# Kernel optimization log

Measured on AMD Instinct MI355X. Metric: run time of the kernel, lower is better.

The kernel has to match this reference:

```python
import jax, jax.numpy as jnp
import numpy as np

N_NODES = 100000


def gcn_conv(x, src, dst, W, b):
    """PyG GCNConv: add self-loops, symmetric D^-1/2 (A+I) D^-1/2 normalization.
    x: [N, Fin]; src/dst: [E'] (self-loops already appended); W: [Fin, Fout]; b: [Fout].
    """
    xw = x @ W  # [N, Fout]
    ones = jnp.ones(dst.shape[0], dtype=x.dtype)
    deg = jax.ops.segment_sum(ones, dst, num_segments=N_NODES)  # in-degree incl. self-loop
    dinv = jnp.where(deg > 0, jax.lax.rsqrt(deg), 0.0)
    norm = dinv[src] * dinv[dst]  # [E']
    msg = xw[src] * norm[:, None]  # gather + scale
    out = jax.ops.segment_sum(msg, dst, num_segments=N_NODES)  # scatter-add
    return out + b


def setup_inputs() -> dict:
    key = jax.random.key(0)
    ks = jax.random.split(key, 12)
    hidden = 64
    E = 1600000
    x_node = jax.random.normal(ks[0], (N_NODES, 1), dtype=jnp.float32)
    edge_index = jax.random.randint(ks[1], (2, E), 0, N_NODES, dtype=jnp.int64)

    def glorot(k, fan_in, fan_out):
        lim = float(np.sqrt(6.0 / (fan_in + fan_out)))
        return jax.random.uniform(k, (fan_in, fan_out), jnp.float32, -lim, lim)

    W1 = glorot(ks[2], 1, hidden)
    b1 = jnp.zeros((hidden,), jnp.float32)
    W2 = glorot(ks[3], hidden, hidden)
    b2 = jnp.zeros((hidden,), jnp.float32)
    W3 = glorot(ks[4], hidden, hidden)
    b3 = jnp.zeros((hidden,), jnp.float32)
    W4 = glorot(ks[5], hidden, 1)
    b4 = jnp.zeros((1,), jnp.float32)
    return {"x_node": x_node, "edge_index": edge_index,
            "W1": W1, "b1": b1, "W2": W2, "b2": b2,
            "W3": W3, "b3": b3, "W4": W4, "b4": b4}


def reference(x_node, edge_index, W1, b1, W2, b2, W3, b3, W4, b4):
    # Append self-loops once (shared by both GCN layers, as PyG does per-layer with identical result)
    loops = jnp.arange(N_NODES, dtype=edge_index.dtype)
    src = jnp.concatenate([edge_index[0], loops])
    dst = jnp.concatenate([edge_index[1], loops])

    h = jax.nn.silu(gcn_conv(x_node, src, dst, W1, b1))
    h = jax.nn.silu(gcn_conv(h, src, dst, W2, b2))
    h = jax.nn.silu(h @ W3 + b3)
    return h @ W4 + b4  # [N, 1]
```

## Files before the change

### kernel.cpp

```cpp
#include <hip/hip_runtime.h>
#include <math.h>

#define N_NODES 100000
#define NPB    392
#define NBUCK  256
#define CAP    7168
#define CHUNKA 4096

#define NCHEB  12
#define SMAX   6.0f

__device__ __forceinline__ float silu_f(float x) {
    return x * __builtin_amdgcn_rcpf(1.0f + __builtin_amdgcn_exp2f(-1.442695041f * x));
}

__global__ __launch_bounds__(512) void k_bucket(const int* __restrict__ src,
                                                const int* __restrict__ dst,
                                                int* __restrict__ gcur,
                                                unsigned int* __restrict__ buf,
                                                const float* __restrict__ W1,
                                                const float* __restrict__ b1,
                                                float* __restrict__ cheb, int E) {
    __shared__ unsigned hist[256];
    __shared__ unsigned gbase[256];
    __shared__ unsigned lcur[256];
    const int t = threadIdx.x;
    if (t < 256) hist[t] = 0;
    __syncthreads();
    const int e0 = blockIdx.x * CHUNKA;
    const int e1 = min(e0 + CHUNKA, E);

    int sR[8], dR[8], bR[8];
#pragma unroll
    for (int q = 0; q < 8; ++q) {
        int e = e0 + t + q * 512;
        if (e < e1) {
            dR[q] = dst[e];
            sR[q] = src[e];
            bR[q] = dR[q] / NPB;
            atomicAdd(&hist[bR[q]], 1u);
        } else bR[q] = -1;
    }
    __syncthreads();
    if (t < 256) {
        unsigned v = hist[t];
        gbase[t] = v ? (unsigned)atomicAdd(&gcur[t], (int)v) : 0u;
        lcur[t] = 0;
    }
    __syncthreads();
#pragma unroll
    for (int q = 0; q < 8; ++q) {
        if (bR[q] >= 0) {
            int b = bR[q];
            unsigned gp = gbase[b] + atomicAdd(&lcur[b], 1u);
            if (gp < CAP)
                buf[(size_t)b * CAP + gp] =
                    ((unsigned)sR[q] << 9) | (unsigned)(dR[q] - b * NPB);
        }
    }

    if (blockIdx.x == 0 && t < 64) {
        int f = t;
        float w = W1[f], b = b1[f];
        float g[NCHEB], th[NCHEB];
        const float pi = 3.14159265358979f;
#pragma unroll
        for (int j = 0; j < NCHEB; ++j) {
            th[j] = (j + 0.5f) * (pi / NCHEB);
            float S = SMAX * __cosf(th[j]);
            float y = fmaf(w, S, b);
            g[j] = y / (1.0f + expf(-y));
        }
#pragma unroll
        for (int k = 0; k < NCHEB; ++k) {
            float s = 0.f;
#pragma unroll
            for (int j = 0; j < NCHEB; ++j)
                s += g[j] * __cosf((float)k * th[j]);
            cheb[k * 64 + f] = s * ((k == 0) ? (1.0f / NCHEB) : (2.0f / NCHEB));
        }
    }
}

__global__ __launch_bounds__(512) void k_deg(const int* __restrict__ gcur,
                                             const unsigned int* __restrict__ buf,
                                             const float* __restrict__ x,
                                             const float* __restrict__ W2,
                                             const float* __restrict__ cheb,
                                             float* __restrict__ cw2,
                                             int* __restrict__ cnt,
                                             float* __restrict__ dinv,
                                             float* __restrict__ xs, int N) {
    __shared__ unsigned hist[512];
    const int b = blockIdx.x, t = threadIdx.x;
    const int cb = min(gcur[b], CAP);
    const unsigned int* bb = buf + (size_t)b * CAP;
    hist[t] = 0;
    __syncthreads();
    for (int i = t; i < cb; i += 512) atomicAdd(&hist[bb[i] & 511u], 1u);
    __syncthreads();
    const int n0 = b * NPB;
    const int np = min(N - n0, NPB);
    if (t < np) {
        cnt[n0 + t] = (int)hist[t];
        float dv = rsqrtf((float)(hist[t] + 1u));
        dinv[n0 + t] = dv;
        xs[n0 + t] = x[n0 + t] * dv;
    }

    if (b == 0 && t < 64) {
        const int f2 = t;
        float acc[NCHEB];
#pragma unroll
        for (int k = 0; k < NCHEB; ++k) acc[k] = 0.f;
        for (int f = 0; f < 64; ++f) {
            float w = W2[f * 64 + f2];
#pragma unroll
            for (int k = 0; k < NCHEB; ++k)
                acc[k] = fmaf(cheb[k * 64 + f], w, acc[k]);
        }
#pragma unroll
        for (int k = 0; k < NCHEB; ++k) cw2[k * 64 + f2] = acc[k];
    }
}

__global__ __launch_bounds__(512) void k_csr3(const int* __restrict__ gcur,
                                              const unsigned int* __restrict__ buf,
                                              const int* __restrict__ cnt,
                                              const float* __restrict__ xs,
                                              const float* __restrict__ dinv,
                                              int* __restrict__ rowptr,
                                              int* __restrict__ csr,
                                              float2* __restrict__ sd, int N) {
    __shared__ unsigned cur[512];
    __shared__ unsigned wtot[8];
    __shared__ unsigned lsrc[CAP];
    __shared__ float    lval[CAP];
    const int b = blockIdx.x, t = threadIdx.x;
    const int lane = t & 63, wid = t >> 6;
    const int cb = min(gcur[b], CAP);
    const unsigned int* bb = buf + (size_t)b * CAP;
    const int n0 = b * NPB;
    const int node = n0 + t;

    unsigned v = (t < NPB && node < N) ? (unsigned)cnt[node] : 0u;
    unsigned sc = v;
#pragma unroll
    for (int off = 1; off < 64; off <<= 1) {
        unsigned y = __shfl_up(sc, off, 64);
        if (lane >= off) sc += y;
    }
    if (lane == 63) wtot[wid] = sc;
    __syncthreads();
    unsigned add = 0;
    for (int w = 0; w < wid; ++w) add += wtot[w];
    unsigned ex = sc - v + add;
    cur[t] = ex;
    __syncthreads();

    int i = t;
    for (; i + 1536 < cb; i += 2048) {
        unsigned p0 = bb[i], p1 = bb[i + 512], p2 = bb[i + 1024], p3 = bb[i + 1536];
        float a0 = xs[p0 >> 9], a1 = xs[p1 >> 9], a2 = xs[p2 >> 9], a3 = xs[p3 >> 9];
        unsigned q0 = atomicAdd(&cur[p0 & 511u], 1u);
        unsigned q1 = atomicAdd(&cur[p1 & 511u], 1u);
        unsigned q2 = atomicAdd(&cur[p2 & 511u], 1u);
        unsigned q3 = atomicAdd(&cur[p3 & 511u], 1u);
        lsrc[q0] = p0 >> 9; lval[q0] = a0;
        lsrc[q1] = p1 >> 9; lval[q1] = a1;
        lsrc[q2] = p2 >> 9; lval[q2] = a2;
        lsrc[q3] = p3 >> 9; lval[q3] = a3;
    }
    for (; i < cb; i += 512) {
        unsigned p = bb[i];
        float a = xs[p >> 9];
        unsigned q = atomicAdd(&cur[p & 511u], 1u);
        lsrc[q] = p >> 9; lval[q] = a;
    }
    __syncthreads();

    for (int j = t; j < cb; j += 512) csr[(size_t)b * CAP + j] = lsrc[j];

    if (t < NPB && node < N) {
        int deg = (int)v;
        int st  = (int)ex;
        rowptr[node] = b * CAP + st;
        float sum = 0.f;
        for (int j = 0; j < deg; ++j) sum += lval[st + j];
        float dv = dinv[node];
        sd[node] = make_float2((sum + xs[node]) * dv, dv);
    }
}

__global__ __launch_bounds__(512) void k_momlp(
    const int* __restrict__ rowptr, const int* __restrict__ cnt,
    const int* __restrict__ csr, const float2* __restrict__ sd,
    const float* __restrict__ cw2,
    const float* __restrict__ b2,
    const float* __restrict__ W3, const float* __restrict__ b3,
    const float* __restrict__ W4, const float* __restrict__ b4,
    float* __restrict__ out, int N)
{
    __shared__ float sA[64 * 65];
    __shared__ float sM[64 * 13];
    __shared__ float sD[64];
    __shared__ float sP[8 * 64];

    const int t = threadIdx.x;
    const int lane = t & 63;
    const int wid  = __builtin_amdgcn_readfirstlane(t >> 6);
    const int nbase = blockIdx.x * 64;
    const int loc = t >> 3, sub = t & 7;
    const int i = nbase + loc;

    int start = 0, deg = 0;
    float2 self = make_float2(0.f, 0.f);
    if (i < N) {
        start = rowptr[i];
        deg   = cnt[i];
        self  = sd[i];
    }

    float m[NCHEB];
    {
        float d = (sub == 0) ? self.y : 0.f;
        float tt = fminf(fmaxf(self.x * (1.0f / SMAX), -1.f), 1.f);
        float t2 = tt + tt, Tm = 1.f, Tc = tt;
        m[0] = d;
        m[1] = d * tt;
#pragma unroll
        for (int k = 2; k < NCHEB; ++k) {
            float Tn = fmaf(t2, Tc, -Tm);
            m[k] = d * Tn;
            Tm = Tc; Tc = Tn;
        }
    }

    int uu[4];
    float2 sv[4];
#pragma unroll
    for (int q = 0; q < 4; ++q) {
        int j = sub + 8 * q;
        uu[q] = (j < deg) ? csr[start + j] : -1;
    }
#pragma unroll
    for (int q = 0; q < 4; ++q)
        sv[q] = (uu[q] >= 0) ? sd[uu[q]] : make_float2(0.f, 0.f);
#pragma unroll
    for (int q = 0; q < 4; ++q) {
        if (uu[q] >= 0) {
            float d = sv[q].y;
            float tt = fminf(fmaxf(sv[q].x * (1.0f / SMAX), -1.f), 1.f);
            float t2 = tt + tt, Tm = 1.f, Tc = tt;
            m[0] += d;
            m[1] = fmaf(d, tt, m[1]);
#pragma unroll
            for (int k = 2; k < NCHEB; ++k) {
                float Tn = fmaf(t2, Tc, -Tm);
                m[k] = fmaf(d, Tn, m[k]);
                Tm = Tc; Tc = Tn;
            }
        }
    }
    for (int j = sub + 32; j < deg; j += 8) {
        int u = csr[start + j];
        float2 su = sd[u];
        float d = su.y;
        float tt = fminf(fmaxf(su.x * (1.0f / SMAX), -1.f), 1.f);
        float t2 = tt + tt, Tm = 1.f, Tc = tt;
        m[0] += d;
        m[1] = fmaf(d, tt, m[1]);
#pragma unroll
        for (int k = 2; k < NCHEB; ++k) {
            float Tn = fmaf(t2, Tc, -Tm);
            m[k] = fmaf(d, Tn, m[k]);
            Tm = Tc; Tc = Tn;
        }
    }
#pragma unroll
    for (int k = 0; k < NCHEB; ++k) {
        m[k] += __shfl_xor(m[k], 1, 64);
        m[k] += __shfl_xor(m[k], 2, 64);
        m[k] += __shfl_xor(m[k], 4, 64);
    }
    sM[loc * 13 + sub] = m[sub];
    if (sub < 4) sM[loc * 13 + 8 + sub] = m[8 + sub];
    if (sub == 0) sD[loc] = self.y;

    float cw[NCHEB];
#pragma unroll
    for (int k = 0; k < NCHEB; ++k) cw[k] = cw2[k * 64 + lane];
    const float b2l = b2[lane];
    __syncthreads();

    const int r0 = wid * 8;
#pragma unroll
    for (int nl = 0; nl < 8; ++nl) {
        int row = r0 + nl;
        float acc = 0.f;
#pragma unroll
        for (int k = 0; k < NCHEB; ++k)
            acc = fmaf(cw[k], sM[row * 13 + k], acc);
        sA[row * 65 + lane] = silu_f(fmaf(sD[row], acc, b2l));
    }
    __syncthreads();

    const int f0 = wid * 8;
    float acc3[8];
#pragma unroll
    for (int j = 0; j < 8; ++j) acc3[j] = b3[f0 + j];
    for (int k = 0; k < 64; ++k) {
        float uv = sA[lane * 65 + k];
#pragma unroll
        for (int j = 0; j < 8; ++j)
            acc3[j] = fmaf(uv, W3[k * 64 + f0 + j], acc3[j]);
    }
    float part = 0.f;
#pragma unroll
    for (int j = 0; j < 8; ++j)
        part = fmaf(silu_f(acc3[j]), W4[f0 + j], part);
    sP[wid * 64 + lane] = part;
    __syncthreads();

    if (wid == 0) {
        int i2 = nbase + lane;
        if (i2 < N) {
            float s = sP[lane];
#pragma unroll
            for (int w = 1; w < 8; ++w) s += sP[w * 64 + lane];
            out[i2] = s + b4[0];
        }
    }
}

extern "C" void kernel_launch(void* const* d_in, const int* in_sizes, int n_in,
                              void* d_out, int out_size, void* d_ws, size_t ws_size,
                              hipStream_t stream) {
    const float* x  = (const float*)d_in[0];
    const int* edge = (const int*)d_in[1];
    const float* W1 = (const float*)d_in[2];
    const float* b1 = (const float*)d_in[3];
    const float* W2 = (const float*)d_in[4];
    const float* b2 = (const float*)d_in[5];
    const float* W3 = (const float*)d_in[6];
    const float* b3 = (const float*)d_in[7];
    const float* W4 = (const float*)d_in[8];
    const float* b4 = (const float*)d_in[9];
    float* out = (float*)d_out;

    const int N = N_NODES;
    const int E = in_sizes[1] / 2;
    const int* src = edge;
    const int* dst = edge + E;
    const int NCHUNK = (E + CHUNKA - 1) / CHUNKA;

    char* ws = (char*)d_ws;
    size_t off = 0;
    int*    gcur   = (int*)(ws + off);    off += 256 * 4;
    float*  dinv   = (float*)(ws + off);  off += (size_t)N * 4;
    float*  xs     = (float*)(ws + off);  off += (size_t)N * 4;
    int*    rowptr = (int*)(ws + off);    off += (size_t)N * 4;
    int*    cnt    = (int*)(ws + off);    off += (size_t)N * 4;
    float2* sd     = (float2*)(ws + off); off += (size_t)N * 8;
    float*  cheb   = (float*)(ws + off);  off += NCHEB * 64 * 4;
    float*  cw2    = (float*)(ws + off);  off += NCHEB * 64 * 4;
    unsigned int* buf = (unsigned int*)(ws + off); off += (size_t)NBUCK * CAP * 4;
    int*    csr    = (int*)(ws + off);    off += (size_t)NBUCK * CAP * 4;

    hipMemsetAsync(gcur, 0, 256 * 4, stream);

    k_bucket<<<NCHUNK, 512, 0, stream>>>(src, dst, gcur, buf, W1, b1, cheb, E);
    k_deg   <<<NBUCK, 512, 0, stream>>>(gcur, buf, x, W2, cheb, cw2, cnt, dinv, xs, N);
    k_csr3  <<<NBUCK, 512, 0, stream>>>(gcur, buf, cnt, xs, dinv,
                                        rowptr, csr, sd, N);
    k_momlp <<<(N + 63) / 64, 512, 0, stream>>>(rowptr, cnt, csr, sd, cw2,
                                                b2, W3, b3, W4, b4, out, N);
}
```

Baseline: 148.7 us.

## Fold degree counting into bucketing via global atomics and drop k_deg kernel

Per-node in-degree is now counted with a global atomicAdd in the bucketing kernel, so the separate degree-histogram kernel is removed. The CSR kernel recomputes the normalized source value from x and cnt on the fly, and also takes over the cw2 precompute. This removes one launch and one full pass over the bucket buffer, but adds about 1.7M global atomics spread across 100K counters and an extra gather of cnt per edge. The memset now also clears the count array.

After: 203.6 us. +36.9%, slower.

```diff
diff --git a/kernel.cpp b/kernel.cpp
--- a/kernel.cpp
+++ b/kernel.cpp
@@ -17,6 +17,7 @@
 __global__ __launch_bounds__(512) void k_bucket(const int* __restrict__ src,
                                                 const int* __restrict__ dst,
                                                 int* __restrict__ gcur,
+                                                int* __restrict__ cnt,
                                                 unsigned int* __restrict__ buf,
                                                 const float* __restrict__ W1,
                                                 const float* __restrict__ b1,
@@ -39,6 +40,7 @@
             sR[q] = src[e];
             bR[q] = dR[q] / NPB;
             atomicAdd(&hist[bR[q]], 1u);
+            atomicAdd(&cnt[dR[q]], 1);
         } else bR[q] = -1;
     }
     __syncthreads();
@@ -82,53 +84,13 @@
     }
 }
 
-__global__ __launch_bounds__(512) void k_deg(const int* __restrict__ gcur,
-                                             const unsigned int* __restrict__ buf,
-                                             const float* __restrict__ x,
-                                             const float* __restrict__ W2,
-                                             const float* __restrict__ cheb,
-                                             float* __restrict__ cw2,
-                                             int* __restrict__ cnt,
-                                             float* __restrict__ dinv,
-                                             float* __restrict__ xs, int N) {
-    __shared__ unsigned hist[512];
-    const int b = blockIdx.x, t = threadIdx.x;
-    const int cb = min(gcur[b], CAP);
-    const unsigned int* bb = buf + (size_t)b * CAP;
-    hist[t] = 0;
-    __syncthreads();
-    for (int i = t; i < cb; i += 512) atomicAdd(&hist[bb[i] & 511u], 1u);
-    __syncthreads();
-    const int n0 = b * NPB;
-    const int np = min(N - n0, NPB);
-    if (t < np) {
-        cnt[n0 + t] = (int)hist[t];
-        float dv = rsqrtf((float)(hist[t] + 1u));
-        dinv[n0 + t] = dv;
-        xs[n0 + t] = x[n0 + t] * dv;
-    }
-
-    if (b == 0 && t < 64) {
-        const int f2 = t;
-        float acc[NCHEB];
-#pragma unroll
-        for (int k = 0; k < NCHEB; ++k) acc[k] = 0.f;
-        for (int f = 0; f < 64; ++f) {
-            float w = W2[f * 64 + f2];
-#pragma unroll
-            for (int k = 0; k < NCHEB; ++k)
-                acc[k] = fmaf(cheb[k * 64 + f], w, acc[k]);
-        }
-#pragma unroll
-        for (int k = 0; k < NCHEB; ++k) cw2[k * 64 + f2] = acc[k];
-    }
-}
-
-__global__ __launch_bounds__(512) void k_csr3(const int* __restrict__ gcur,
+__global__ __launch_bounds__(512) void k_csr4(const int* __restrict__ gcur,
                                               const unsigned int* __restrict__ buf,
                                               const int* __restrict__ cnt,
-                                              const float* __restrict__ xs,
-                                              const float* __restrict__ dinv,
+                                              const float* __restrict__ x,
+                                              const float* __restrict__ W2,
+                                              const float* __restrict__ cheb,
+                                              float* __restrict__ cw2,
                                               int* __restrict__ rowptr,
                                               int* __restrict__ csr,
                                               float2* __restrict__ sd, int N) {
@@ -161,21 +123,28 @@
     int i = t;
     for (; i + 1536 < cb; i += 2048) {
         unsigned p0 = bb[i], p1 = bb[i + 512], p2 = bb[i + 1024], p3 = bb[i + 1536];
-        float a0 = xs[p0 >> 9], a1 = xs[p1 >> 9], a2 = xs[p2 >> 9], a3 = xs[p3 >> 9];
+        int s0 = p0 >> 9, s1 = p1 >> 9, s2 = p2 >> 9, s3 = p3 >> 9;
+        float x0 = x[s0], x1 = x[s1], x2 = x[s2], x3 = x[s3];
+        int c0 = cnt[s0], c1 = cnt[s1], c2 = cnt[s2], c3 = cnt[s3];
+        float a0 = x0 * rsqrtf((float)(c0 + 1));
+        float a1 = x1 * rsqrtf((float)(c1 + 1));
+        float a2 = x2 * rsqrtf((float)(c2 + 1));
+        float a3 = x3 * rsqrtf((float)(c3 + 1));
         unsigned q0 = atomicAdd(&cur[p0 & 511u], 1u);
         unsigned q1 = atomicAdd(&cur[p1 & 511u], 1u);
         unsigned q2 = atomicAdd(&cur[p2 & 511u], 1u);
         unsigned q3 = atomicAdd(&cur[p3 & 511u], 1u);
-        lsrc[q0] = p0 >> 9; lval[q0] = a0;
-        lsrc[q1] = p1 >> 9; lval[q1] = a1;
-        lsrc[q2] = p2 >> 9; lval[q2] = a2;
-        lsrc[q3] = p3 >> 9; lval[q3] = a3;
+        lsrc[q0] = (unsigned)s0; lval[q0] = a0;
+        lsrc[q1] = (unsigned)s1; lval[q1] = a1;
+        lsrc[q2] = (unsigned)s2; lval[q2] = a2;
+        lsrc[q3] = (unsigned)s3; lval[q3] = a3;
     }
     for (; i < cb; i += 512) {
         unsigned p = bb[i];
-        float a = xs[p >> 9];
+        int s = p >> 9;
+        float a = x[s] * rsqrtf((float)(cnt[s] + 1));
         unsigned q = atomicAdd(&cur[p & 511u], 1u);
-        lsrc[q] = p >> 9; lval[q] = a;
+        lsrc[q] = (unsigned)s; lval[q] = a;
     }
     __syncthreads();
 
@@ -185,10 +154,25 @@
         int deg = (int)v;
         int st  = (int)ex;
         rowptr[node] = b * CAP + st;
+        float dv = rsqrtf((float)(deg + 1));
         float sum = 0.f;
         for (int j = 0; j < deg; ++j) sum += lval[st + j];
-        float dv = dinv[node];
-        sd[node] = make_float2((sum + xs[node]) * dv, dv);
+        sd[node] = make_float2((sum + x[node] * dv) * dv, dv);
+    }
+
+    if (b == 0 && t < 64) {
+        const int f2 = t;
+        float acc[NCHEB];
+#pragma unroll
+        for (int k = 0; k < NCHEB; ++k) acc[k] = 0.f;
+        for (int f = 0; f < 64; ++f) {
+            float w = W2[f * 64 + f2];
+#pragma unroll
+            for (int k = 0; k < NCHEB; ++k)
+                acc[k] = fmaf(cheb[k * 64 + f], w, acc[k]);
+        }
+#pragma unroll
+        for (int k = 0; k < NCHEB; ++k) cw2[k * 64 + f2] = acc[k];
     }
 }
 
@@ -357,21 +341,18 @@
     char* ws = (char*)d_ws;
     size_t off = 0;
     int*    gcur   = (int*)(ws + off);    off += 256 * 4;
-    float*  dinv   = (float*)(ws + off);  off += (size_t)N * 4;
-    float*  xs     = (float*)(ws + off);  off += (size_t)N * 4;
+    int*    cnt    = (int*)(ws + off);    off += (size_t)N * 4;
     int*    rowptr = (int*)(ws + off);    off += (size_t)N * 4;
-    int*    cnt    = (int*)(ws + off);    off += (size_t)N * 4;
     float2* sd     = (float2*)(ws + off); off += (size_t)N * 8;
     float*  cheb   = (float*)(ws + off);  off += NCHEB * 64 * 4;
     float*  cw2    = (float*)(ws + off);  off += NCHEB * 64 * 4;
     unsigned int* buf = (unsigned int*)(ws + off); off += (size_t)NBUCK * CAP * 4;
     int*    csr    = (int*)(ws + off);    off += (size_t)NBUCK * CAP * 4;
 
-    hipMemsetAsync(gcur, 0, 256 * 4, stream);
-
-    k_bucket<<<NCHUNK, 512, 0, stream>>>(src, dst, gcur, buf, W1, b1, cheb, E);
-    k_deg   <<<NBUCK, 512, 0, stream>>>(gcur, buf, x, W2, cheb, cw2, cnt, dinv, xs, N);
-    k_csr3  <<<NBUCK, 512, 0, stream>>>(gcur, buf, cnt, xs, dinv,
+    hipMemsetAsync(gcur, 0, (256 + (size_t)N) * 4, stream);
+
+    k_bucket<<<NCHUNK, 512, 0, stream>>>(src, dst, gcur, cnt, buf, W1, b1, cheb, E);
+    k_csr4  <<<NBUCK, 512, 0, stream>>>(gcur, buf, cnt, x, W2, cheb, cw2,
                                         rowptr, csr, sd, N);
     k_momlp <<<(N + 63) / 64, 512, 0, stream>>>(rowptr, cnt, csr, sd, cw2,
                                                 b2, W3, b3, W4, b4, out, N);
```
